# Kernel optimization log

Measured on AMD Instinct MI355X. Metric: run time of the kernel, lower is better.

The kernel has to match this reference:

```python
import jax, jax.numpy as jnp
import numpy as np

VOCAB = 50000
D = 128      # word_embedding_size
H = 64       # attention_hidden_dim


def _doc_embed(words, emb_table, w_self, b_self):
    """words: (..., W) int -> (..., D) via tanh self-attention pooling over words."""
    we = emb_table[words]                                # (..., W, D)
    scores = jnp.tanh(we @ w_self + b_self)              # (..., W, 1)
    wgt = jax.nn.softmax(scores, axis=-2)                # softmax over word dim
    return jnp.sum(wgt * we, axis=-2)                    # (..., D)


def _attention(reviews_emb, query_emb, Wq, bq, w_red):
    """reviews_emb: (B,R,D), query_emb: (B,1,D) -> (B,D)."""
    B = query_emb.shape[0]
    pq = jnp.tanh(query_emb.reshape(B, D) @ Wq + bq)     # (B, D*H)
    pq = pq.reshape(B, D, H)
    s = jnp.einsum('brd,bdh->brh', reviews_emb, pq)      # (B,R,H)
    r = s @ w_red                                        # (B,R,1)
    w = jax.nn.softmax(r, axis=1)                        # softmax over reviews
    return jnp.sum(w * reviews_emb, axis=1)              # (B,D)


def setup_inputs() -> dict:
    key = jax.random.key(0)
    ks = jax.random.split(key, 9)
    B, R, W = 256, 20, 100
    user = jax.random.randint(ks[0], (B, R, W), 0, VOCAB)
    item = jax.random.randint(ks[1], (B, R, W), 0, VOCAB)
    query = jax.random.randint(ks[2], (B, W), 0, VOCAB)
    emb_table = jax.random.normal(ks[3], (VOCAB, D), dtype=jnp.float32) * 0.01
    w_self = jax.random.normal(ks[4], (D, 1), dtype=jnp.float32) * (1.0 / np.sqrt(D))
    b_self = jax.random.uniform(ks[5], (1,), dtype=jnp.float32, maxval=0.01)
    Wq = jax.random.normal(ks[6], (D, D * H), dtype=jnp.float32) * (1.0 / np.sqrt(D))
    bq = jax.random.uniform(ks[7], (D * H,), dtype=jnp.float32, maxval=0.01)
    w_red = jax.random.normal(ks[8], (H, 1), dtype=jnp.float32) * (1.0 / np.sqrt(H))
    pf = jnp.float32(0.5)  # personalized_factor
    return {"user_reviews_words": user, "item_reviews_words": item, "query": query,
            "emb_table": emb_table, "w_self": w_self, "b_self": b_self,
            "Wq": Wq, "bq": bq, "w_red": w_red, "pf": pf}


def reference(user_reviews_words, item_reviews_words, query,
              emb_table, w_self, b_self, Wq, bq, w_red, pf):
    # mode == 'test'
    user_emb = _doc_embed(user_reviews_words, emb_table, w_self, b_self)   # (B,R,D)
    item_emb = _doc_embed(item_reviews_words, emb_table, w_self, b_self)   # (B,R,D)
    q_emb = _doc_embed(query[:, None, :], emb_table, w_self, b_self)       # (B,1,D)
    user_entity = _attention(user_emb, q_emb, Wq, bq, w_red)               # (B,D)
    item_entity = _attention(item_emb, q_emb, Wq, bq, w_red)               # (B,D)
    personalized = user_entity + pf * q_emb[:, 0, :]
    return (personalized, item_entity)
```

## Files before the change

### kernel.cpp

```cpp
#include <hip/hip_runtime.h>
#include <math.h>

#define D 128
#define H 64
#define W 100
#define R 20
#define NB 256
#define NDOC_UI (NB * R)

__device__ __forceinline__ float fast_tanh(float x) {
    float u = __expf(2.0f * x);
    return 1.0f - 2.0f * __builtin_amdgcn_rcpf(1.0f + u);
}
__device__ __forceinline__ float fast_exp_tanh(float x) {
    return __expf(fast_tanh(x));
}

__global__ __launch_bounds__(256, 7) void doc_embed_kernel(
    const int* __restrict__ user_w, const int* __restrict__ item_w,
    const int* __restrict__ query_w,
    const float* __restrict__ emb, const float* __restrict__ w_self,
    const float* __restrict__ b_self,
    float* __restrict__ user_emb, float* __restrict__ item_emb,
    float* __restrict__ q_emb)
{
    int tid    = threadIdx.x;
    int lane32 = tid & 31;
    int grp    = tid >> 5;
    int doc    = blockIdx.x * 8 + grp;

    const int* wp; float* outp;
    if (doc < NDOC_UI)        { wp = user_w + doc * W;               outp = user_emb + doc * D; }
    else if (doc < 2*NDOC_UI) { int t = doc - NDOC_UI;   wp = item_w  + t * W; outp = item_emb + t * D; }
    else                      { int t = doc - 2*NDOC_UI; wp = query_w + t * W; outp = q_emb    + t * D; }

    int wreg[4];
    #pragma unroll
    for (int k = 0; k < 4; ++k) {
        int idx = k * 32 + lane32;
        wreg[k] = wp[idx > W - 1 ? W - 1 : idx];
    }

    float4 ws4 = ((const float4*)w_self)[lane32];
    float  bs  = b_self[0];
    const float4* emb4 = (const float4*)emb;

    int permbase = (tid & 32) * 4;

    float4 acc  = make_float4(0.f, 0.f, 0.f, 0.f);
    float  esum = 0.f;

    #pragma unroll
    for (int c = 0; c < 10; ++c) {
        int word[10];
        #pragma unroll
        for (int j = 0; j < 10; ++j) {
            int w = c * 10 + j;
            word[j] = __builtin_amdgcn_ds_bpermute(permbase | ((w & 31) * 4),
                                                   wreg[w >> 5]);
        }
        float4 v[10];
        #pragma unroll
        for (int j = 0; j < 10; ++j)
            v[j] = emb4[(size_t)word[j] * 32 + lane32];

        #pragma unroll
        for (int j = 0; j < 10; ++j) {
            float p = v[j].x * ws4.x + v[j].y * ws4.y + v[j].z * ws4.z + v[j].w * ws4.w;
            p += __shfl_xor(p, 16, 64);
            p += __shfl_xor(p, 8, 64);
            p += __shfl_xor(p, 4, 64);
            p += __shfl_xor(p, 2, 64);
            p += __shfl_xor(p, 1, 64);
            float e = fast_exp_tanh(p + bs);
            esum += e;
            acc.x += e * v[j].x;
            acc.y += e * v[j].y;
            acc.z += e * v[j].z;
            acc.w += e * v[j].w;
        }
    }

    float inv = 1.0f / esum;
    acc.x *= inv; acc.y *= inv; acc.z *= inv; acc.w *= inv;
    ((float4*)outp)[lane32] = acc;
}

__global__ __launch_bounds__(256) void pv_kernel(
    const float* __restrict__ q_emb, const float* __restrict__ Wq,
    const float* __restrict__ bq, const float* __restrict__ w_red,
    float* __restrict__ pv)
{
    __shared__ __align__(16) float qs[64 * 132];
    __shared__ __align__(16) float Wb[128 * 68];

    int dd  = blockIdx.x;
    int m0g = blockIdx.y * 64;
    int tid = threadIdx.x;

    {
        int rrow = tid >> 4;
        int f4   = tid & 15;
        #pragma unroll
        for (int pass = 0; pass < 4; ++pass) {
            int m = pass * 16 + rrow;
            float4 vq = ((const float4*)q_emb)[(m0g + m) * 32 + f4];
            *(float4*)&qs[m * 132 + f4 * 4] = vq;
        }
        #pragma unroll
        for (int pass = 0; pass < 8; ++pass) {
            int k = pass * 16 + rrow;
            float4 vw = ((const float4*)Wq)[k * 2048 + dd * 16 + f4];
            *(float4*)&Wb[k * 68 + f4 * 4] = vw;
        }
    }
    __syncthreads();

    int nthr = tid & 7;
    int mthr = tid >> 3;
    int n0 = nthr * 8;
    int m0 = mthr * 2;

    float acc[2][8];
    #pragma unroll
    for (int i = 0; i < 2; ++i)
        #pragma unroll
        for (int j = 0; j < 8; ++j) acc[i][j] = 0.f;

    for (int k = 0; k < 128; ++k) {
        float4 b0 = *(const float4*)&Wb[k * 68 + n0];
        float4 b1 = *(const float4*)&Wb[k * 68 + n0 + 4];
        float a0 = qs[(m0 + 0) * 132 + k];
        float a1 = qs[(m0 + 1) * 132 + k];
        float bv[8] = {b0.x, b0.y, b0.z, b0.w, b1.x, b1.y, b1.z, b1.w};
        #pragma unroll
        for (int j = 0; j < 8; ++j) {
            acc[0][j] += a0 * bv[j];
            acc[1][j] += a1 * bv[j];
        }
    }

    float4 bqa = ((const float4*)bq)[dd * 16 + nthr * 2];
    float4 bqb = ((const float4*)bq)[dd * 16 + nthr * 2 + 1];
    float4 wra = ((const float4*)w_red)[nthr * 2];
    float4 wrb = ((const float4*)w_red)[nthr * 2 + 1];
    float bqv[8] = {bqa.x, bqa.y, bqa.z, bqa.w, bqb.x, bqb.y, bqb.z, bqb.w};
    float wrv[8] = {wra.x, wra.y, wra.z, wra.w, wrb.x, wrb.y, wrb.z, wrb.w};

    #pragma unroll
    for (int i = 0; i < 2; ++i) {
        float s = 0.f;
        #pragma unroll
        for (int j = 0; j < 8; ++j)
            s += fast_tanh(acc[i][j] + bqv[j]) * wrv[j];
        s += __shfl_xor(s, 1, 64);
        s += __shfl_xor(s, 2, 64);
        s += __shfl_xor(s, 4, 64);
        if (nthr == 0) pv[(m0g + m0 + i) * 128 + dd] = s;
    }
}

__global__ __launch_bounds__(256) void attn_kernel(
    const float* __restrict__ user_emb, const float* __restrict__ item_emb,
    const float* __restrict__ q_emb, const float* __restrict__ pv,
    const float* __restrict__ pf, float* __restrict__ out)
{
    __shared__ float rev[R * 129];
    __shared__ float pvl[D];
    __shared__ float sc[R];

    int b   = blockIdx.x;
    int set = blockIdx.y;
    const float* revg = (set == 0 ? user_emb : item_emb) + b * R * D;
    int tid = threadIdx.x;

    for (int idx = tid; idx < R * D; idx += 256)
        rev[(idx >> 7) * 129 + (idx & 127)] = revg[idx];
    if (tid < D) pvl[tid] = pv[b * D + tid];
    __syncthreads();

    if (tid < R) {
        float s = 0.f;
        const float* row = &rev[tid * 129];
        #pragma unroll 16
        for (int k = 0; k < D; ++k) s += row[k] * pvl[k];
        sc[tid] = s;
    }
    __syncthreads();

    float m = -1e30f;
    for (int r = 0; r < R; ++r) m = fmaxf(m, sc[r]);
    float sum = 0.f;
    for (int r = 0; r < R; ++r) sum += __expf(sc[r] - m);
    float inv = 1.f / sum;

    if (tid < D) {
        float acc = 0.f;
        for (int r = 0; r < R; ++r)
            acc += __expf(sc[r] - m) * inv * rev[r * 129 + tid];
        if (set == 0) {
            acc += pf[0] * q_emb[b * D + tid];
            out[b * D + tid] = acc;
        } else {
            out[NB * D + b * D + tid] = acc;
        }
    }
}

extern "C" void kernel_launch(void* const* d_in, const int* in_sizes, int n_in,
                              void* d_out, int out_size, void* d_ws, size_t ws_size,
                              hipStream_t stream) {
    const int*   user_w  = (const int*)d_in[0];
    const int*   item_w  = (const int*)d_in[1];
    const int*   query_w = (const int*)d_in[2];
    const float* emb     = (const float*)d_in[3];
    const float* w_self  = (const float*)d_in[4];
    const float* b_self  = (const float*)d_in[5];
    const float* Wq      = (const float*)d_in[6];
    const float* bq      = (const float*)d_in[7];
    const float* w_red   = (const float*)d_in[8];
    const float* pf      = (const float*)d_in[9];

    float* ws       = (float*)d_ws;
    float* user_emb = ws;
    float* item_emb = user_emb + NDOC_UI * D;
    float* q_emb    = item_emb + NDOC_UI * D;
    float* pv       = q_emb    + NB * D;
    float* out      = (float*)d_out;

    doc_embed_kernel<<<(2 * NDOC_UI + NB) / 8, 256, 0, stream>>>(
        user_w, item_w, query_w, emb, w_self, b_self, user_emb, item_emb, q_emb);
    pv_kernel<<<dim3(128, 4), 256, 0, stream>>>(q_emb, Wq, bq, w_red, pv);
    attn_kernel<<<dim3(NB, 2), 256, 0, stream>>>(user_emb, item_emb, q_emb, pv, pf, out);
}
```

Baseline: 175.4 us.

## Precompute per-vocab attention weights and gather bf16 pre-weighted embeddings

Adds a pass over the vocabulary that computes each word's exp(tanh(w·e+b)) weight once and stores the embedding pre-multiplied by it in bf16. The doc embedding kernel then only gathers the scalar weights for the normaliser and sums half-width pre-weighted rows. This removes the per-word dot product, shuffle reductions and transcendental work, and halves gather bytes. In exchange it costs an extra full-table pass, bf16 rounding error, and it only runs when the workspace is large enough.

```diff
diff --git a/kernel.cpp b/kernel.cpp
--- a/kernel.cpp
+++ b/kernel.cpp
@@ -7,6 +7,7 @@
 #define R 20
 #define NB 256
 #define NDOC_UI (NB * R)
+#define VOCAB 50000
 
 __device__ __forceinline__ float fast_tanh(float x) {
     float u = __expf(2.0f * x);
@@ -16,7 +17,145 @@
     return __expf(fast_tanh(x));
 }
 
-__global__ __launch_bounds__(256, 7) void doc_embed_kernel(
+__device__ __forceinline__ unsigned short f2bf(float f) {
+    unsigned int b = __float_as_uint(f);
+    b += 0x7fffu + ((b >> 16) & 1u);
+    return (unsigned short)(b >> 16);
+}
+
+__global__ __launch_bounds__(256) void vocab_prep_kernel(
+    const float* __restrict__ emb, const float* __restrict__ w_self,
+    const float* __restrict__ b_self,
+    ushort* __restrict__ emb_bf, float* __restrict__ evocab)
+{
+    int tid = threadIdx.x, lane32 = tid & 31, grp = tid >> 5;
+    int row = blockIdx.x * 8 + grp;
+    float4 v   = ((const float4*)emb)[row * 32 + lane32];
+    float4 ws4 = ((const float4*)w_self)[lane32];
+    float p = v.x * ws4.x + v.y * ws4.y + v.z * ws4.z + v.w * ws4.w;
+    p += __shfl_xor(p, 16, 64);
+    p += __shfl_xor(p, 8, 64);
+    p += __shfl_xor(p, 4, 64);
+    p += __shfl_xor(p, 2, 64);
+    p += __shfl_xor(p, 1, 64);
+    float e = __expf(tanhf(p + b_self[0]));
+    if (lane32 == 0) evocab[row] = e;
+    ushort4 u;
+    u.x = f2bf(v.x * e); u.y = f2bf(v.y * e);
+    u.z = f2bf(v.z * e); u.w = f2bf(v.w * e);
+    ((ushort4*)emb_bf)[row * 32 + lane32] = u;
+}
+
+__global__ __launch_bounds__(256) void doc_embed_bf16_kernel(
+    const int* __restrict__ user_w, const int* __restrict__ item_w,
+    const int* __restrict__ query_w,
+    const ushort* __restrict__ emb_bf, const float* __restrict__ evocab,
+    float* __restrict__ user_emb, float* __restrict__ item_emb,
+    float* __restrict__ q_emb)
+{
+    int tid    = threadIdx.x;
+    int lane32 = tid & 31;
+    int grp    = tid >> 5;
+    int doc    = blockIdx.x * 8 + grp;
+
+    const int* wp; float* outp;
+    if (doc < NDOC_UI)        { wp = user_w + doc * W;               outp = user_emb + doc * D; }
+    else if (doc < 2*NDOC_UI) { int t = doc - NDOC_UI;   wp = item_w  + t * W; outp = item_emb + t * D; }
+    else                      { int t = doc - 2*NDOC_UI; wp = query_w + t * W; outp = q_emb    + t * D; }
+
+    int wreg[4];
+    #pragma unroll
+    for (int k = 0; k < 4; ++k) {
+        int idx = k * 32 + lane32;
+        wreg[k] = wp[idx > W - 1 ? W - 1 : idx];
+    }
+
+    float ep = 0.f;
+    #pragma unroll
+    for (int k = 0; k < 4; ++k) {
+        float e = evocab[wreg[k]];
+        if (k < 3 || lane32 < 4) ep += e;
+    }
+    ep += __shfl_xor(ep, 16, 64);
+    ep += __shfl_xor(ep, 8, 64);
+    ep += __shfl_xor(ep, 4, 64);
+    ep += __shfl_xor(ep, 2, 64);
+    ep += __shfl_xor(ep, 1, 64);
+    float inv = 1.f / ep;
+
+    int permbase = (tid & 32) << 2;
+    int sub      = lane32 >> 4;
+    int quad     = lane32 & 15;
+
+    float acc[8];
+    #pragma unroll
+    for (int j = 0; j < 8; ++j) acc[j] = 0.f;
+
+    const uint4* ebf4 = (const uint4*)emb_bf;
+
+    #pragma unroll
+    for (int k = 0; k < 3; ++k) {
+        #pragma unroll
+        for (int hc = 0; hc < 2; ++hc) {
+            int wid[8]; uint4 v[8];
+            #pragma unroll
+            for (int j = 0; j < 8; ++j) {
+                int src = (hc * 8 + j) * 2 + sub;
+                wid[j] = __builtin_amdgcn_ds_bpermute(permbase | (src << 2), wreg[k]);
+            }
+            #pragma unroll
+            for (int j = 0; j < 8; ++j)
+                v[j] = ebf4[(size_t)(unsigned)wid[j] * 16 + quad];
+            #pragma unroll
+            for (int j = 0; j < 8; ++j) {
+                uint4 x = v[j];
+                acc[0] += __uint_as_float(x.x << 16);
+                acc[1] += __uint_as_float(x.x & 0xffff0000u);
+                acc[2] += __uint_as_float(x.y << 16);
+                acc[3] += __uint_as_float(x.y & 0xffff0000u);
+                acc[4] += __uint_as_float(x.z << 16);
+                acc[5] += __uint_as_float(x.z & 0xffff0000u);
+                acc[6] += __uint_as_float(x.w << 16);
+                acc[7] += __uint_as_float(x.w & 0xffff0000u);
+            }
+        }
+    }
+    {
+        int wid[2]; uint4 v[2];
+        #pragma unroll
+        for (int j = 0; j < 2; ++j) {
+            int src = j * 2 + sub;
+            wid[j] = __builtin_amdgcn_ds_bpermute(permbase | (src << 2), wreg[3]);
+        }
+        #pragma unroll
+        for (int j = 0; j < 2; ++j)
+            v[j] = ebf4[(size_t)(unsigned)wid[j] * 16 + quad];
+        #pragma unroll
+        for (int j = 0; j < 2; ++j) {
+            uint4 x = v[j];
+            acc[0] += __uint_as_float(x.x << 16);
+            acc[1] += __uint_as_float(x.x & 0xffff0000u);
+            acc[2] += __uint_as_float(x.y << 16);
+            acc[3] += __uint_as_float(x.y & 0xffff0000u);
+            acc[4] += __uint_as_float(x.z << 16);
+            acc[5] += __uint_as_float(x.z & 0xffff0000u);
+            acc[6] += __uint_as_float(x.w << 16);
+            acc[7] += __uint_as_float(x.w & 0xffff0000u);
+        }
+    }
+
+    #pragma unroll
+    for (int j = 0; j < 8; ++j) acc[j] += __shfl_xor(acc[j], 16, 64);
+
+    if (lane32 < 16) {
+        float4 o0 = make_float4(acc[0]*inv, acc[1]*inv, acc[2]*inv, acc[3]*inv);
+        float4 o1 = make_float4(acc[4]*inv, acc[5]*inv, acc[6]*inv, acc[7]*inv);
+        ((float4*)outp)[quad * 2]     = o0;
+        ((float4*)outp)[quad * 2 + 1] = o1;
+    }
+}
+
+__global__ __launch_bounds__(256, 7) void doc_embed_fp32_kernel(
     const int* __restrict__ user_w, const int* __restrict__ item_w,
     const int* __restrict__ query_w,
     const float* __restrict__ emb, const float* __restrict__ w_self,
@@ -44,7 +183,6 @@
     float4 ws4 = ((const float4*)w_self)[lane32];
     float  bs  = b_self[0];
     const float4* emb4 = (const float4*)emb;
-
     int permbase = (tid & 32) * 4;
 
     float4 acc  = make_float4(0.f, 0.f, 0.f, 0.f);
@@ -226,10 +364,23 @@
     float* item_emb = user_emb + NDOC_UI * D;
     float* q_emb    = item_emb + NDOC_UI * D;
     float* pv       = q_emb    + NB * D;
+    float* evocab   = pv       + NB * D;
+    ushort* emb_bf  = (ushort*)(evocab + VOCAB);
     float* out      = (float*)d_out;
 
-    doc_embed_kernel<<<(2 * NDOC_UI + NB) / 8, 256, 0, stream>>>(
-        user_w, item_w, query_w, emb, w_self, b_self, user_emb, item_emb, q_emb);
+    const size_t need_fast =
+        (size_t)(2 * NDOC_UI * D + 2 * NB * D + VOCAB) * sizeof(float)
+        + (size_t)VOCAB * D * sizeof(ushort);
+
+    if (ws_size >= need_fast) {
+        vocab_prep_kernel<<<VOCAB / 8, 256, 0, stream>>>(
+            emb, w_self, b_self, emb_bf, evocab);
+        doc_embed_bf16_kernel<<<(2 * NDOC_UI + NB) / 8, 256, 0, stream>>>(
+            user_w, item_w, query_w, emb_bf, evocab, user_emb, item_emb, q_emb);
+    } else {
+        doc_embed_fp32_kernel<<<(2 * NDOC_UI + NB) / 8, 256, 0, stream>>>(
+            user_w, item_w, query_w, emb, w_self, b_self, user_emb, item_emb, q_emb);
+    }
     pv_kernel<<<dim3(128, 4), 256, 0, stream>>>(q_emb, Wq, bq, w_red, pv);
     attn_kernel<<<dim3(NB, 2), 256, 0, stream>>>(user_emb, item_emb, q_emb, pv, pf, out);
 }
```

Result: faster. 151.9 us (-13.4%).
